# Kernel optimization log

Measured on AMD Instinct MI355X. Metric: run time of the kernel, lower is better.

## Reference

```python
import jax, jax.numpy as jnp
import numpy as np

SIGMA = 1.0
LN2 = 0.6931471805599453


def _raster_mask(kd, kh, kw, include_center):
    # PixelCNN-style causal mask in (depth, h, w) raster order
    idx = np.arange(kd * kh * kw).reshape(kd, kh, kw)
    c = (kd * kh * kw) // 2
    m = (idx <= c) if include_center else (idx < c)
    return jnp.asarray(m, jnp.float32)[None, None]  # [1,1,kd,kh,kw] (OIDHW broadcast)


def _conv3d(x, w, b, padding):
    y = jax.lax.conv_general_dilated(x, w, (1, 1, 1), padding,
                                     dimension_numbers=('NCDHW', 'OIDHW', 'NCDHW'))
    return y + b[None, :, None, None, None]


def _quantize1d(x, centers):
    # distances of every element to every center: [..., L]
    d = (x[..., None] - centers) ** 2
    phi_soft = jax.nn.softmax(-SIGMA * d, axis=-1)
    qsoft = jnp.einsum('...l,l->...', phi_soft, centers)
    symbols = jnp.argmin(d, axis=-1)  # int32 hard assignment
    qhard = centers[symbols]
    return qsoft, qhard, symbols


def setup_inputs() -> dict:
    key = jax.random.key(0)
    ks = jax.random.split(key, 8)
    N, H, W, C = 4, 128, 128, 16
    K, L = 24, 6
    s = 0.05
    return {
        'x': jax.random.normal(ks[0], (N, H, W, C), jnp.float32),
        'centers': jax.random.uniform(ks[1], (L,), jnp.float32, -2.0, 2.0),
        'w0': jax.random.normal(ks[2], (K, 1, 3, 3, 3), jnp.float32) * s,
        'b0': jnp.zeros((K,), jnp.float32),
        'w1': jax.random.normal(ks[3], (K, K, 3, 3, 3), jnp.float32) * s,
        'b1': jnp.zeros((K,), jnp.float32),
        'w2': jax.random.normal(ks[4], (K, K, 3, 3, 3), jnp.float32) * s,
        'b2': jnp.zeros((K,), jnp.float32),
        'w_out': jax.random.normal(ks[5], (L, K, 1, 1, 1), jnp.float32) * s,
        'b_out': jnp.zeros((L,), jnp.float32),
    }


def reference(x, centers, w0, b0, w1, b1, w2, b2, w_out, b_out):
    # ---- soft/hard quantization with straight-through estimator ----
    qsoft, qhard, symbols = _quantize1d(x, centers)
    qbar = qsoft + jax.lax.stop_gradient(qhard - qsoft)  # [N,H,W,C] NHWC

    pc_in = jnp.transpose(qbar, (0, 3, 1, 2))[:, None]      # [N,1,C,H,W] (depth=C)
    tgt = jnp.transpose(symbols, (0, 3, 1, 2))              # [N,C,H,W]

    # pad input volume with pad_value = centers[0] (causal boundary symbol)
    pad_value = centers[0].astype(pc_in.dtype)
    v = jax.lax.pad(pc_in, pad_value,
                    [(0, 0, 0), (0, 0, 0), (1, 1, 0), (1, 1, 0), (1, 1, 0)])

    mask_a = _raster_mask(3, 3, 3, include_center=False)
    mask_b = _raster_mask(3, 3, 3, include_center=True)

    # res_shallow: masked-A conv -> masked-B conv -> masked-B conv + residual -> 1x1x1 logits
    h0 = jax.nn.relu(_conv3d(v, w0 * mask_a, b0, 'VALID'))     # [N,K,C,H,W]
    h1 = jax.nn.relu(_conv3d(h0, w1 * mask_b, b1, 'SAME'))
    h2 = _conv3d(h1, w2 * mask_b, b2, 'SAME') + h0
    logits = _conv3d(jax.nn.relu(h2), w_out, b_out, 'SAME')    # [N,L,C,H,W]

    # per-element bitcost: cross-entropy of hard symbols, in bits
    lp = jax.nn.log_softmax(logits, axis=1)
    bc = -jnp.take_along_axis(lp, tgt[:, None], axis=1)[:, 0] / LN2  # [N,C,H,W]
    bc_train = jnp.transpose(bc, (0, 2, 3, 1))                        # NCHW -> NHWC
    return qbar, bc_train
```

## Files before the change

### kernel.cpp

```cpp
#include <hip/hip_runtime.h>
#include <cstddef>

typedef _Float16 f16;
typedef _Float16 f16x8 __attribute__((ext_vector_type(8)));
typedef float f32x16 __attribute__((ext_vector_type(16)));

#define N_ 4
#define D_ 16
#define H_ 128
#define W_ 128
#define K_ 24
#define L_ 6
#define NTAP_A 13

#define OFF_TGT  0ull
#define OFF_H0   4194304ull
#define OFF_H1   54525952ull
#define OFF_W0P  104857600ull
#define OFF_W1B  104858880ull
#define OFF_W2B  104880384ull

#define AROW_B 6336
#define A_BYTES 120384
#define B_BYTES 21504
#define SMEM_BYTES 141888

__host__ __device__ constexpr int aoff(int p, int c, int g) {
  int idx8 = 2 * c + g;
  int ts = idx8 >= 3 ? 1 : 0;
  int t = 2 * p + ts;
  int cb = idx8 - 3 * ts;
  int dz = t / 9 - 1;
  int rr = t % 9;
  int dy = rr / 3 - 1;
  int dx = rr % 3 - 1;
  int rowb = (dz < 0) ? (dy + 1) : (10 + dy + 1);
  return rowb * AROW_B + (dx + 1) * 48 + cb * 16;
}

__device__ __forceinline__ void quant1(float xv, const float cs[L_],
                                       float& qb, int& sym) {
  float dv[L_];
  float dmin = 3.4e38f;
  sym = 0;
#pragma unroll
  for (int l = 0; l < L_; ++l) {
    float df = xv - cs[l];
    float d = df * df;
    dv[l] = d;
    if (d < dmin) { dmin = d; sym = l; }
  }
  float e[L_];
  float s = 0.f;
#pragma unroll
  for (int l = 0; l < L_; ++l) {
    e[l] = expf(dmin - dv[l]);
    s += e[l];
  }
  float qsoft = 0.f;
#pragma unroll
  for (int l = 0; l < L_; ++l) qsoft += (e[l] / s) * cs[l];
  qb = qsoft + (cs[sym] - qsoft);
}

__global__ __launch_bounds__(256) void qbar_pack_k(
    const float* __restrict__ x, const float* __restrict__ centers,
    float* __restrict__ qbar_out,
    const float* __restrict__ w0, const float* __restrict__ w1,
    const float* __restrict__ w2, float* __restrict__ w0p,
    f16* __restrict__ w1B, f16* __restrict__ w2B) {
  int idx = blockIdx.x * 256 + threadIdx.x;

  float cs[L_];
#pragma unroll
  for (int l = 0; l < L_; ++l) cs[l] = centers[l];

  float qb; int sym;
  quant1(x[idx], cs, qb, sym);
  qbar_out[idx] = qb;

  if (blockIdx.x < 8) {
    int gid = blockIdx.x * 256 + threadIdx.x;
    for (int i = gid; i < NTAP_A * K_; i += 2048) {
      int co = i % K_;
      int t  = i / K_;
      w0p[t * K_ + co] = w0[co * 27 + t];
    }
    for (int i = gid; i < 2 * 10752; i += 2048) {
      int sel = i / 10752;
      int idx2 = i % 10752;
      int chunk = idx2 / 512;
      int r = idx2 % 512;
      int g = r / 256;
      int nn = (r % 256) / 8;
      int j = r % 8;
      int p = chunk / 3, c = chunk % 3;
      int idx8 = 2 * c + g;
      int ts = idx8 >= 3 ? 1 : 0;
      int t = 2 * p + ts;
      int ci = (idx8 - 3 * ts) * 8 + j;
      const float* w = sel ? w2 : w1;
      float v = (nn < K_) ? w[(nn * K_ + ci) * 27 + t] : 0.f;
      (sel ? w2B : w1B)[idx2] = (f16)v;
    }
  }
}

__global__ __launch_bounds__(256, 2) void conv0_fused_k(
    const float* __restrict__ x, const float* __restrict__ centers,
    const float* __restrict__ w0p, const float* __restrict__ b0,
    f16* __restrict__ h0, int* __restrict__ tgt) {
  __shared__ float qs[19 * 132];
  __shared__ f16 eo[1024 * K_];

  int blk = blockIdx.x;
  int hb = blk & 15;
  int d = (blk >> 4) & 15;
  int n = blk >> 8;
  int h_base = hb * 8;

  float cs[L_];
#pragma unroll
  for (int l = 0; l < L_; ++l) cs[l] = centers[l];
  float pv = cs[0];

  for (int i = threadIdx.x; i < 19 * 130; i += 256) {
    int r = i / 130, s = i % 130;
    int dd = (r < 10) ? d - 1 : d;
    int hh = h_base - 1 + ((r < 10) ? r : r - 10);
    int ww = s - 1;
    float qv = pv;
    int sym = 0;
    bool in = (dd >= 0) && ((unsigned)hh < (unsigned)H_) &&
              ((unsigned)ww < (unsigned)W_);
    if (in) {
      float xv = x[((n * H_ + hh) * W_ + ww) * D_ + dd];
      quant1(xv, cs, qv, sym);
    }
    qs[r * 132 + s] = qv;
    if (r >= 11 && (unsigned)ww < (unsigned)W_)
      tgt[((n * D_ + d) * H_ + (h_base + r - 11)) * W_ + ww] = sym;
  }
  __syncthreads();

  float bia[K_];
#pragma unroll
  for (int co = 0; co < K_; ++co) bia[co] = b0[co];

#pragma unroll 1
  for (int k = 0; k < 4; ++k) {
    int p = threadIdx.x + 256 * k;
    int rl = p >> 7;
    int wl = p & 127;

    float acc[K_];
#pragma unroll
    for (int co = 0; co < K_; ++co) acc[co] = bia[co];

#pragma unroll
    for (int t = 0; t < NTAP_A; ++t) {
      int r, s;
      if (t < 9)       { r = rl + t / 3; s = wl + t % 3; }
      else if (t < 12) { r = rl + 10;    s = wl + (t - 9); }
      else             { r = rl + 11;    s = wl; }
      float xv = qs[r * 132 + s];
      const float* wr = w0p + t * K_;
#pragma unroll
      for (int co = 0; co < K_; ++co) acc[co] = fmaf(xv, wr[co], acc[co]);
    }

    union { f16 hv[K_]; uint4 u[3]; } u;
#pragma unroll
    for (int co = 0; co < K_; ++co) u.hv[co] = (f16)fmaxf(acc[co], 0.f);
    uint4* ep = (uint4*)(eo + p * K_);
    ep[0] = u.u[0]; ep[1] = u.u[1]; ep[2] = u.u[2];
  }
  __syncthreads();

  {
    uint4* g = (uint4*)(h0 + (size_t)((n * D_ + d) * H_ + h_base) * (W_ * K_));
    const uint4* s = (const uint4*)eo;
    for (int i = threadIdx.x; i < 3072; i += 256) g[i] = s[i];
  }
}

__device__ __forceinline__ void conv_core8(const f16* __restrict__ src,
                                           const f16* __restrict__ wB,
                                           char* smem, int n, int d, int h_base,
                                           f32x16& acc0, f32x16& acc1) {
  const int tid = threadIdx.x;
  for (int i = tid; i < 7296; i += 1024) {
    int r = i / 384, qq = i % 384;
    int dd = (r < 10) ? d - 1 : d;
    int hh = h_base - 1 + ((r < 10) ? r : r - 10);
    uint4 v = make_uint4(0, 0, 0, 0);
    if (dd >= 0 && (unsigned)hh < (unsigned)H_)
      v = ((const uint4*)(src + (size_t)((n * D_ + dd) * H_ + hh) * 3072))[qq];
    *(uint4*)(smem + r * AROW_B + 48 + qq * 16) = v;
  }
  if (tid < 114) {
    int r = tid / 6, k = tid % 6;
    int byte = r * AROW_B + (k < 3 ? k * 16 : 6192 + (k - 3) * 16);
    *(uint4*)(smem + byte) = make_uint4(0, 0, 0, 0);
  }
  {
    const uint4* g = (const uint4*)wB;
    uint4* s = (uint4*)(smem + A_BYTES);
    for (int i = tid; i < 1344; i += 1024) s[i] = g[i];
  }
  __syncthreads();

  const int lane = tid & 63;
  const int wv = tid >> 6;
  const int m = lane & 31;
  const int g01 = lane >> 5;

  const int hs = wv >> 1;
  const int wc0 = (wv & 1) * 64;
  const char* Ab0 = smem + hs * AROW_B + (wc0 + m) * 48;
  const char* Ab1 = Ab0 + 32 * 48;
  const char* Bb = smem + A_BYTES + g01 * 512 + m * 16;

#pragma unroll
  for (int r = 0; r < 16; ++r) { acc0[r] = 0.f; acc1[r] = 0.f; }

#pragma unroll
  for (int p = 0; p < 7; ++p) {
#pragma unroll
    for (int c = 0; c < 3; ++c) {
      const int C0 = aoff(p, c, 0);
      const int C1 = aoff(p, c, 1);
      int off = g01 ? C1 : C0;
      f16x8 b = *(const f16x8*)(Bb + (p * 3 + c) * 1024);
      f16x8 a0 = *(const f16x8*)(Ab0 + off);
      f16x8 a1 = *(const f16x8*)(Ab1 + off);
      acc0 = __builtin_amdgcn_mfma_f32_32x32x16_f16(a0, b, acc0, 0, 0, 0);
      acc1 = __builtin_amdgcn_mfma_f32_32x32x16_f16(a1, b, acc1, 0, 0, 0);
    }
  }
}

__global__ __launch_bounds__(1024, 1) void conv1_mfma_k(
    const f16* __restrict__ src, const f16* __restrict__ wB,
    const float* __restrict__ bias, f16* __restrict__ dst) {
  __shared__ __align__(16) char smem[SMEM_BYTES];

  int blk = blockIdx.x;
  int hb = blk & 15;
  int d = (blk >> 4) & 15;
  int n = blk >> 8;
  int h_base = hb * 8;

  f32x16 acc0, acc1;
  conv_core8(src, wB, smem, n, d, h_base, acc0, acc1);

  const int lane = threadIdx.x & 63;
  const int wv = threadIdx.x >> 6;
  const int m = lane & 31;
  const int g01 = lane >> 5;

  __syncthreads();
  f16* ldsE = (f16*)smem;
  if (m < K_) {
    float bv = bias[m];
#pragma unroll
    for (int tt = 0; tt < 2; ++tt) {
      const f32x16& A = tt ? acc1 : acc0;
#pragma unroll
      for (int r = 0; r < 16; ++r) {
        int mrow = (r & 3) + 8 * (r >> 2) + 4 * g01;
        int pos = (2 * wv + tt) * 32 + mrow;
        ldsE[pos * K_ + m] = (f16)fmaxf(A[r] + bv, 0.f);
      }
    }
  }
  __syncthreads();
  {
    uint4* g = (uint4*)(dst + (size_t)((n * D_ + d) * H_ + h_base) * 3072);
    const uint4* s = (const uint4*)smem;
    for (int i = threadIdx.x; i < 3072; i += 1024) g[i] = s[i];
  }
}

__global__ __launch_bounds__(1024, 1) void conv2_mfma_k(
    const f16* __restrict__ h1, const f16* __restrict__ h0,
    const f16* __restrict__ wB, const float* __restrict__ bias,
    const float* __restrict__ w_out, const float* __restrict__ b_out,
    const int* __restrict__ tgt, float* __restrict__ bco) {
  __shared__ __align__(16) char smem[SMEM_BYTES];

  int blk = blockIdx.x;
  int hb = blk & 15;
  int d = (blk >> 4) & 15;
  int n = blk >> 8;
  int h_base = hb * 8;

  f32x16 acc0, acc1;
  conv_core8(h1, wB, smem, n, d, h_base, acc0, acc1);

  const int lane = threadIdx.x & 63;
  const int wv = threadIdx.x >> 6;
  const int m = lane & 31;
  const int g01 = lane >> 5;

  __syncthreads();
  float* Ef = (float*)smem;
  if (m < K_) {
    float bv = bias[m];
#pragma unroll
    for (int tt = 0; tt < 2; ++tt) {
      const f32x16& A = tt ? acc1 : acc0;
#pragma unroll
      for (int r = 0; r < 16; ++r) {
        int mrow = (r & 3) + 8 * (r >> 2) + 4 * g01;
        int pos = (2 * wv + tt) * 32 + mrow;
        Ef[pos * 28 + m] = A[r] + bv;
      }
    }
  }
  __syncthreads();

  {
    int pos = threadIdx.x;
    int hh = h_base + (pos >> 7);
    int w = pos & 127;

    size_t gpos = (size_t)((n * D_ + d) * H_ + h_base) * W_ + pos;
    const f16x8* hp = (const f16x8*)(h0 + gpos * K_);
    f16x8 e0 = hp[0], e1 = hp[1], e2 = hp[2];

    const float* ef = Ef + pos * 28;
    float vals[K_];
#pragma unroll
    for (int k = 0; k < K_; ++k) {
      float h0v = (float)(k < 8 ? e0[k] : (k < 16 ? e1[k - 8] : e2[k - 16]));
      vals[k] = fmaxf(ef[k] + h0v, 0.f);
    }

    float lg[L_];
#pragma unroll
    for (int l = 0; l < L_; ++l) lg[l] = b_out[l];
#pragma unroll
    for (int k = 0; k < K_; ++k) {
      float rv = vals[k];
#pragma unroll
      for (int l = 0; l < L_; ++l) lg[l] = fmaf(rv, w_out[l * K_ + k], lg[l]);
    }
    float mm = lg[0];
#pragma unroll
    for (int l = 1; l < L_; ++l) mm = fmaxf(mm, lg[l]);
    float s = 0.f;
#pragma unroll
    for (int l = 0; l < L_; ++l) s += expf(lg[l] - mm);

    int t = tgt[gpos];
    float lt = lg[0];
#pragma unroll
    for (int l = 1; l < L_; ++l) lt = (t == l) ? lg[l] : lt;

    float lp = lt - mm - logf(s);
    bco[(size_t)((n * H_ + hh) * W_ + w) * D_ + d] = -lp / 0.69314718055994530942f;
  }
}

extern "C" void kernel_launch(void* const* d_in, const int* in_sizes, int n_in,
                              void* d_out, int out_size, void* d_ws, size_t ws_size,
                              hipStream_t stream) {
  const float* x       = (const float*)d_in[0];
  const float* centers = (const float*)d_in[1];
  const float* w0      = (const float*)d_in[2];
  const float* b0      = (const float*)d_in[3];
  const float* w1      = (const float*)d_in[4];
  const float* b1      = (const float*)d_in[5];
  const float* w2      = (const float*)d_in[6];
  const float* b2      = (const float*)d_in[7];
  const float* w_out   = (const float*)d_in[8];
  const float* b_out   = (const float*)d_in[9];
  float* out = (float*)d_out;

  char* ws = (char*)d_ws;
  int*   tg   = (int*)(ws + OFF_TGT);
  f16*   h0f  = (f16*)(ws + OFF_H0);
  f16*   h1f  = (f16*)(ws + OFF_H1);
  float* w0p  = (float*)(ws + OFF_W0P);
  f16*   w1B  = (f16*)(ws + OFF_W1B);
  f16*   w2B  = (f16*)(ws + OFF_W2B);

  hipLaunchKernelGGL(qbar_pack_k, dim3(4096), dim3(256), 0, stream,
                     x, centers, out, w0, w1, w2, w0p, w1B, w2B);
  hipLaunchKernelGGL(conv0_fused_k, dim3(1024), dim3(256), 0, stream,
                     x, centers, w0p, b0, h0f, tg);
  hipLaunchKernelGGL(conv1_mfma_k, dim3(1024), dim3(1024), 0, stream,
                     h0f, w1B, b1, h1f);
  hipLaunchKernelGGL(conv2_mfma_k, dim3(1024), dim3(1024), 0, stream,
                     h1f, h0f, w2B, b2, w_out, b_out, tg, out + 1048576);
}
```

Baseline: 207.3 us.

## Quantize once into planar fp16 buffer and simplify conv0 to read it

The quantization kernel now computes qbar, symbols and a depth-planar fp16 copy of qbar once per element with vectorized loads, transposed through shared memory. The conv0 kernel reads this compact fp16 buffer instead of re-quantizing strided NHWC input with halo recomputation, and writes h0 directly to global memory instead of staging through shared memory. Weight packing is spread across blocks instead of being looped in the first eight. This adds a 2 MB intermediate buffer round trip and makes h0 stores less coalesced, in exchange for removing redundant quantization and the uncoalesced depth-strided reads.

```diff
diff --git a/kernel.cpp b/kernel.cpp
--- a/kernel.cpp
+++ b/kernel.cpp
@@ -14,11 +14,12 @@
 #define NTAP_A 13
 
 #define OFF_TGT  0ull
-#define OFF_H0   4194304ull
-#define OFF_H1   54525952ull
-#define OFF_W0P  104857600ull
-#define OFF_W1B  104858880ull
-#define OFF_W2B  104880384ull
+#define OFF_Q16  4194304ull
+#define OFF_H0   6291456ull
+#define OFF_H1   56623104ull
+#define OFF_W0P  106954752ull
+#define OFF_W1B  106956800ull
+#define OFF_W2B  106978304ull
 
 #define AROW_B 6336
 #define A_BYTES 120384
@@ -63,83 +64,104 @@
   qb = qsoft + (cs[sym] - qsoft);
 }
 
-__global__ __launch_bounds__(256) void qbar_pack_k(
+__global__ __launch_bounds__(256) void quant_all_k(
     const float* __restrict__ x, const float* __restrict__ centers,
-    float* __restrict__ qbar_out,
+    float* __restrict__ qbar_out, f16* __restrict__ q16,
+    int* __restrict__ tgt,
     const float* __restrict__ w0, const float* __restrict__ w1,
     const float* __restrict__ w2, float* __restrict__ w0p,
     f16* __restrict__ w1B, f16* __restrict__ w2B) {
-  int idx = blockIdx.x * 256 + threadIdx.x;
+  __shared__ f16 q16s[2048];
+  __shared__ int syms[2048];
+
+  int blk = blockIdx.x;
+  int n = blk >> 7;
+  int h = blk & 127;
+  int t = threadIdx.x;
 
   float cs[L_];
 #pragma unroll
   for (int l = 0; l < L_; ++l) cs[l] = centers[l];
 
-  float qb; int sym;
-  quant1(x[idx], cs, qb, sym);
-  qbar_out[idx] = qb;
-
-  if (blockIdx.x < 8) {
-    int gid = blockIdx.x * 256 + threadIdx.x;
-    for (int i = gid; i < NTAP_A * K_; i += 2048) {
-      int co = i % K_;
-      int t  = i / K_;
-      w0p[t * K_ + co] = w0[co * 27 + t];
-    }
-    for (int i = gid; i < 2 * 10752; i += 2048) {
-      int sel = i / 10752;
-      int idx2 = i % 10752;
-      int chunk = idx2 / 512;
-      int r = idx2 % 512;
-      int g = r / 256;
-      int nn = (r % 256) / 8;
-      int j = r % 8;
-      int p = chunk / 3, c = chunk % 3;
-      int idx8 = 2 * c + g;
-      int ts = idx8 >= 3 ? 1 : 0;
-      int t = 2 * p + ts;
-      int ci = (idx8 - 3 * ts) * 8 + j;
-      const float* w = sel ? w2 : w1;
-      float v = (nn < K_) ? w[(nn * K_ + ci) * 27 + t] : 0.f;
-      (sel ? w2B : w1B)[idx2] = (f16)v;
-    }
-  }
-}
-
-__global__ __launch_bounds__(256, 2) void conv0_fused_k(
-    const float* __restrict__ x, const float* __restrict__ centers,
+  const float4* x4 = (const float4*)x + (size_t)blk * 512;
+  float4* o4 = (float4*)qbar_out + (size_t)blk * 512;
+
+  int w = t >> 1;
+  int c0 = (t & 1) * 8;
+#pragma unroll
+  for (int e = 0; e < 2; ++e) {
+    float4 v = x4[2 * t + e];
+    float4 o;
+    float qb; int sym;
+    quant1(v.x, cs, qb, sym); o.x = qb;
+    q16s[(c0 + 4 * e + 0) * 128 + w] = (f16)qb; syms[(c0 + 4 * e + 0) * 128 + w] = sym;
+    quant1(v.y, cs, qb, sym); o.y = qb;
+    q16s[(c0 + 4 * e + 1) * 128 + w] = (f16)qb; syms[(c0 + 4 * e + 1) * 128 + w] = sym;
+    quant1(v.z, cs, qb, sym); o.z = qb;
+    q16s[(c0 + 4 * e + 2) * 128 + w] = (f16)qb; syms[(c0 + 4 * e + 2) * 128 + w] = sym;
+    quant1(v.w, cs, qb, sym); o.w = qb;
+    q16s[(c0 + 4 * e + 3) * 128 + w] = (f16)qb; syms[(c0 + 4 * e + 3) * 128 + w] = sym;
+    o4[2 * t + e] = o;
+  }
+  __syncthreads();
+
+  for (int i = t; i < 2048; i += 256) {
+    int dd = i >> 7, ww = i & 127;
+    size_t g = ((size_t)(n * D_ + dd) * H_ + h) * W_ + ww;
+    q16[g] = q16s[i];
+    tgt[g] = syms[i];
+  }
+
+  int pid = blk * 256 + t;
+  if (pid < NTAP_A * K_) {
+    int co = pid % K_;
+    int tt = pid / K_;
+    w0p[tt * K_ + co] = w0[co * 27 + tt];
+  } else if (pid < NTAP_A * K_ + 2 * 10752) {
+    int i2 = pid - NTAP_A * K_;
+    int sel = i2 / 10752;
+    int idx2 = i2 % 10752;
+    int chunk = idx2 / 512;
+    int r = idx2 % 512;
+    int g = r / 256;
+    int nn = (r % 256) / 8;
+    int j = r % 8;
+    int p = chunk / 3, cc = chunk % 3;
+    int idx8 = 2 * cc + g;
+    int ts = idx8 >= 3 ? 1 : 0;
+    int tp = 2 * p + ts;
+    int ci = (idx8 - 3 * ts) * 8 + j;
+    const float* wsrc = sel ? w2 : w1;
+    float v = (nn < K_) ? wsrc[(nn * K_ + ci) * 27 + tp] : 0.f;
+    (sel ? w2B : w1B)[idx2] = (f16)v;
+  }
+}
+
+__global__ __launch_bounds__(256) void conv0_q16_k(
+    const f16* __restrict__ q16, const float* __restrict__ centers,
     const float* __restrict__ w0p, const float* __restrict__ b0,
-    f16* __restrict__ h0, int* __restrict__ tgt) {
-  __shared__ float qs[19 * 132];
-  __shared__ f16 eo[1024 * K_];
+    f16* __restrict__ h0) {
+  __shared__ f16 qs[2 * 6 * 132];
 
   int blk = blockIdx.x;
-  int hb = blk & 15;
-  int d = (blk >> 4) & 15;
-  int n = blk >> 8;
-  int h_base = hb * 8;
-
-  float cs[L_];
-#pragma unroll
-  for (int l = 0; l < L_; ++l) cs[l] = centers[l];
-  float pv = cs[0];
-
-  for (int i = threadIdx.x; i < 19 * 130; i += 256) {
-    int r = i / 130, s = i % 130;
-    int dd = (r < 10) ? d - 1 : d;
-    int hh = h_base - 1 + ((r < 10) ? r : r - 10);
+  int hb = blk & 31;
+  int d = (blk >> 5) & 15;
+  int n = blk >> 9;
+  int h_base = hb * 4;
+
+  f16 pv16 = (f16)centers[0];
+
+  for (int i = threadIdx.x; i < 1584; i += 256) {
+    int pl = i / 792;
+    int rr = (i / 132) % 6;
+    int s = i % 132;
+    int qp = d - 1 + pl;
+    int hh = h_base - 1 + rr;
     int ww = s - 1;
-    float qv = pv;
-    int sym = 0;
-    bool in = (dd >= 0) && ((unsigned)hh < (unsigned)H_) &&
-              ((unsigned)ww < (unsigned)W_);
-    if (in) {
-      float xv = x[((n * H_ + hh) * W_ + ww) * D_ + dd];
-      quant1(xv, cs, qv, sym);
-    }
-    qs[r * 132 + s] = qv;
-    if (r >= 11 && (unsigned)ww < (unsigned)W_)
-      tgt[((n * D_ + d) * H_ + (h_base + r - 11)) * W_ + ww] = sym;
+    f16 val = pv16;
+    if (qp >= 0 && (unsigned)hh < (unsigned)H_ && (unsigned)ww < (unsigned)W_)
+      val = q16[((size_t)(n * D_ + qp) * H_ + hh) * W_ + ww];
+    qs[i] = val;
   }
   __syncthreads();
 
@@ -147,11 +169,11 @@
 #pragma unroll
   for (int co = 0; co < K_; ++co) bia[co] = b0[co];
 
-#pragma unroll 1
-  for (int k = 0; k < 4; ++k) {
-    int p = threadIdx.x + 256 * k;
-    int rl = p >> 7;
-    int wl = p & 127;
+#pragma unroll
+  for (int k2 = 0; k2 < 2; ++k2) {
+    int pos = threadIdx.x + 256 * k2;
+    int rl = pos >> 7;
+    int w = pos & 127;
 
     float acc[K_];
 #pragma unroll
@@ -159,28 +181,21 @@
 
 #pragma unroll
     for (int t = 0; t < NTAP_A; ++t) {
-      int r, s;
-      if (t < 9)       { r = rl + t / 3; s = wl + t % 3; }
-      else if (t < 12) { r = rl + 10;    s = wl + (t - 9); }
-      else             { r = rl + 11;    s = wl; }
-      float xv = qs[r * 132 + s];
+      int dz, dy, dx;
+      if (t < 9)       { dz = -1; dy = t / 3 - 1; dx = t % 3 - 1; }
+      else if (t < 12) { dz = 0;  dy = -1;        dx = t - 10; }
+      else             { dz = 0;  dy = 0;         dx = -1; }
+      float qv = (float)qs[(dz + 1) * 792 + (rl + dy + 1) * 132 + (w + dx + 1)];
       const float* wr = w0p + t * K_;
 #pragma unroll
-      for (int co = 0; co < K_; ++co) acc[co] = fmaf(xv, wr[co], acc[co]);
+      for (int co = 0; co < K_; ++co) acc[co] = fmaf(qv, wr[co], acc[co]);
     }
 
     union { f16 hv[K_]; uint4 u[3]; } u;
 #pragma unroll
     for (int co = 0; co < K_; ++co) u.hv[co] = (f16)fmaxf(acc[co], 0.f);
-    uint4* ep = (uint4*)(eo + p * K_);
-    ep[0] = u.u[0]; ep[1] = u.u[1]; ep[2] = u.u[2];
-  }
-  __syncthreads();
-
-  {
-    uint4* g = (uint4*)(h0 + (size_t)((n * D_ + d) * H_ + h_base) * (W_ * K_));
-    const uint4* s = (const uint4*)eo;
-    for (int i = threadIdx.x; i < 3072; i += 256) g[i] = s[i];
+    uint4* dst = (uint4*)(h0 + ((size_t)((n * D_ + d) * H_ + h_base + rl) * W_ + w) * K_);
+    dst[0] = u.u[0]; dst[1] = u.u[1]; dst[2] = u.u[2];
   }
 }
 
@@ -380,16 +395,17 @@
 
   char* ws = (char*)d_ws;
   int*   tg   = (int*)(ws + OFF_TGT);
+  f16*   q16  = (f16*)(ws + OFF_Q16);
   f16*   h0f  = (f16*)(ws + OFF_H0);
   f16*   h1f  = (f16*)(ws + OFF_H1);
   float* w0p  = (float*)(ws + OFF_W0P);
   f16*   w1B  = (f16*)(ws + OFF_W1B);
   f16*   w2B  = (f16*)(ws + OFF_W2B);
 
-  hipLaunchKernelGGL(qbar_pack_k, dim3(4096), dim3(256), 0, stream,
-                     x, centers, out, w0, w1, w2, w0p, w1B, w2B);
-  hipLaunchKernelGGL(conv0_fused_k, dim3(1024), dim3(256), 0, stream,
-                     x, centers, w0p, b0, h0f, tg);
+  hipLaunchKernelGGL(quant_all_k, dim3(512), dim3(256), 0, stream,
+                     x, centers, out, q16, tg, w0, w1, w2, w0p, w1B, w2B);
+  hipLaunchKernelGGL(conv0_q16_k, dim3(2048), dim3(256), 0, stream,
+                     q16, centers, w0p, b0, h0f);
   hipLaunchKernelGGL(conv1_mfma_k, dim3(1024), dim3(1024), 0, stream,
                      h0f, w1B, b1, h1f);
   hipLaunchKernelGGL(conv2_mfma_k, dim3(1024), dim3(1024), 0, stream,
```

Result: faster. 200.6 us (-3.2%).
